# Optimization experiments

Measured on AMD Instinct MI355X. Metric: run time of the kernel, lower is better.

## Reference

```python
import jax, jax.numpy as jnp
import numpy as np

B, L, D, N = 4, 8192, 1024, 16


def setup_inputs() -> dict:
    key = jax.random.key(0)
    ks = jax.random.split(key, 6)
    x = jax.random.normal(ks[0], (B, L, D), dtype=jnp.float32)
    Wd = jax.random.normal(ks[1], (D, D), dtype=jnp.float32) / np.sqrt(D).astype(np.float32)
    bd = jnp.zeros((D,), dtype=jnp.float32)
    Wb = jax.random.normal(ks[2], (N, D), dtype=jnp.float32) / np.sqrt(D).astype(np.float32)
    bb = jnp.zeros((N,), dtype=jnp.float32)
    Wc = jax.random.normal(ks[3], (N, D), dtype=jnp.float32) / np.sqrt(D).astype(np.float32)
    bc = jnp.zeros((N,), dtype=jnp.float32)
    # A_log = log(rand*0.9 + 0.1) as in the torch init
    A_log = jnp.log(jax.random.uniform(ks[4], (D, N), dtype=jnp.float32) * 0.9 + 0.1)
    D_param = jnp.ones((D,), dtype=jnp.float32)
    return {"x": x, "Wd": Wd, "bd": bd, "Wb": Wb, "bb": bb,
            "Wc": Wc, "bc": bc, "A_log": A_log, "D_param": D_param}


def _ssm(x, Wd, bd, Wb, bb, Wc, bc, A_log, D_param):
    # Projections over the full sequence (batched GEMMs)
    delta = jax.nn.softplus(jnp.einsum('bld,ed->ble', x, Wd) + bd)   # [B,L,D]
    Bm = jnp.einsum('bld,nd->bln', x, Wb) + bb                       # [B,L,N]
    Cm = jnp.einsum('bld,nd->bln', x, Wc) + bc                       # [B,L,N]
    A = -jnp.exp(A_log)                                              # [D,N]

    h0 = jnp.zeros((x.shape[0], x.shape[2], A_log.shape[1]), dtype=x.dtype)  # [B,D,N]

    def step(h, inp):
        x_t, d_t, b_t, c_t = inp  # [B,D],[B,D],[B,N],[B,N]
        bar_A = jnp.exp(jnp.minimum(d_t[..., None] * A, 2.0))                 # [B,D,N]
        bar_B = jnp.clip(d_t[..., None] * b_t[:, None, :], -2.0, 2.0)         # [B,D,N]
        h = jnp.clip(bar_A * h + bar_B * x_t[..., None], -100.0, 100.0)       # [B,D,N]
        y_t = jnp.sum(h * c_t[:, None, :], axis=-1) + x_t * D_param           # [B,D]
        return h, y_t

    xs = (jnp.swapaxes(x, 0, 1), jnp.swapaxes(delta, 0, 1),
          jnp.swapaxes(Bm, 0, 1), jnp.swapaxes(Cm, 0, 1))  # time-major [L,B,*]
    _, ys = jax.lax.scan(step, h0, xs)  # ys: [L,B,D]
    return jnp.swapaxes(ys, 0, 1)       # [B,L,D]


def reference(x, Wd, bd, Wb, bb, Wc, bc, A_log, D_param):
    return _ssm(x, Wd, bd, Wb, bb, Wc, bc, A_log, D_param)
```

## Files before the change

### kernel.cpp

```cpp
#include <hip/hip_runtime.h>
#include <hip/hip_bf16.h>
#include <cstdint>
#include <cstddef>


#define LOG2E 1.44269504088896340736f

typedef short bf16x8 __attribute__((ext_vector_type(8)));
typedef float f32x4 __attribute__((ext_vector_type(4)));

#if __has_builtin(__builtin_amdgcn_exp2f)
#define EXP2F(x) __builtin_amdgcn_exp2f(x)
#else
#define EXP2F(x) exp2f(x)
#endif

static constexpr int B_ = 4;
static constexpr int L_ = 8192;
static constexpr int CHUNKS = 32;
static constexpr int CHUNK = L_ / CHUNKS;
static constexpr int WARM = 128;


__global__ void cvt_x_kernel(const float* __restrict__ x, __hip_bfloat16* __restrict__ xb) {
    size_t i = ((size_t)blockIdx.x * blockDim.x + threadIdx.x) * 4;
    float4 v = *(const float4*)(x + i);
    __hip_bfloat16* p = xb + i;
    p[0] = __float2bfloat16(v.x);
    p[1] = __float2bfloat16(v.y);
    p[2] = __float2bfloat16(v.z);
    p[3] = __float2bfloat16(v.w);
}

__global__ void prep_wall_kernel(const float* __restrict__ Wd, const float* __restrict__ Wb,
                                 const float* __restrict__ Wc, __hip_bfloat16* __restrict__ Wall) {
    int gid = blockIdx.x * blockDim.x + threadIdx.x;
    size_t idx = (size_t)gid * 4;
    int row = (int)(idx >> 10);
    int k = (int)(idx & 1023);
    __hip_bfloat16* p = Wall + idx;
    const float* src = nullptr;
    if (row < 1024) src = Wd + (size_t)row * 1024 + k;
    else if (row < 1040) src = Wb + (size_t)(row - 1024) * 1024 + k;
    else if (row < 1056) src = Wc + (size_t)(row - 1040) * 1024 + k;
    if (src) {
        float4 v = *(const float4*)src;
        p[0] = __float2bfloat16(v.x);
        p[1] = __float2bfloat16(v.y);
        p[2] = __float2bfloat16(v.z);
        p[3] = __float2bfloat16(v.w);
    } else {
        __hip_bfloat16 z = __float2bfloat16(0.0f);
        p[0] = z; p[1] = z; p[2] = z; p[3] = z;
    }
}


__global__ __launch_bounds__(256) void gemm_kernel(
    const __hip_bfloat16* __restrict__ X, const __hip_bfloat16* __restrict__ W,
    const float* __restrict__ bd, const float* __restrict__ bb, const float* __restrict__ bc,
    __hip_bfloat16* __restrict__ deltab, float* __restrict__ Bm, float* __restrict__ Cm) {
    __shared__ short smem[128 * 144];
    short* As = smem;
    short* Bs = smem + 128 * 64;
    const int bm = blockIdx.x;
    const int bn = blockIdx.y;
    const int t = threadIdx.x;
    const int lane = t & 63;
    const int wave = t >> 6;
    const int wm = (wave >> 1) * 64;
    const int wn = (wave & 1) * 64;
    const int rowS = t >> 3;
    const int kbS = t & 7;

    f32x4 acc[4][4];
#pragma unroll
    for (int i = 0; i < 4; ++i)
#pragma unroll
        for (int j = 0; j < 4; ++j) {
            f32x4 z = {0.f, 0.f, 0.f, 0.f};
            acc[i][j] = z;
        }

    const size_t Abase = (size_t)bm * 128 * 1024;
    const size_t Bbase = (size_t)bn * 128 * 1024;

    for (int kt = 0; kt < 16; ++kt) {
        __syncthreads();
#pragma unroll
        for (int r = 0; r < 4; ++r) {
            int row = r * 32 + rowS;
            int kb = kbS ^ (row & 7);
            const __hip_bfloat16* ga = X + Abase + (size_t)row * 1024 + kt * 64 + kb * 8;
            const __hip_bfloat16* gb = W + Bbase + (size_t)row * 1024 + kt * 64 + kb * 8;
            __builtin_amdgcn_global_load_lds(
                (const __attribute__((address_space(1))) unsigned int*)ga,
                (__attribute__((address_space(3))) unsigned int*)&As[(r * 256 + t) * 8], 16, 0, 0);
            __builtin_amdgcn_global_load_lds(
                (const __attribute__((address_space(1))) unsigned int*)gb,
                (__attribute__((address_space(3))) unsigned int*)&Bs[(r * 256 + t) * 8], 16, 0, 0);
        }
        __syncthreads();
#pragma unroll
        for (int ks = 0; ks < 2; ++ks) {
            bf16x8 af[4], bfr[4];
#pragma unroll
            for (int i = 0; i < 4; ++i) {
                int m = wm + i * 16 + (lane & 15);
                int kb = (ks * 4 + (lane >> 4)) ^ (m & 7);
                af[i] = *(const bf16x8*)&As[m * 64 + kb * 8];
            }
#pragma unroll
            for (int j = 0; j < 4; ++j) {
                int n = wn + j * 16 + (lane & 15);
                int kb = (ks * 4 + (lane >> 4)) ^ (n & 7);
                bfr[j] = *(const bf16x8*)&Bs[n * 64 + kb * 8];
            }
#pragma unroll
            for (int i = 0; i < 4; ++i)
#pragma unroll
                for (int j = 0; j < 4; ++j)
                    acc[i][j] = __builtin_amdgcn_mfma_f32_16x16x32_bf16(af[i], bfr[j], acc[i][j], 0, 0, 0);
        }
    }

    const int rquad = lane >> 4;
    const int cl = lane & 15;
    if (bn < 8) {
        __syncthreads();
#pragma unroll
        for (int i = 0; i < 4; ++i) {
            int row0 = wm + i * 16 + rquad * 4;
#pragma unroll
            for (int j = 0; j < 4; ++j) {
                int col_l = wn + j * 16 + cl;
                float bv = bd[bn * 128 + col_l];
#pragma unroll
                for (int r = 0; r < 4; ++r) {
                    float z = acc[i][j][r] + bv;
                    float sp = fmaxf(z, 0.f) + __logf(1.f + __expf(-fabsf(z)));
                    __hip_bfloat16 hb = __float2bfloat16(sp);
                    smem[(row0 + r) * 144 + col_l] = *(short*)&hb;
                }
            }
        }
        __syncthreads();
        const int rloc = t >> 4;
        const int seg = t & 15;
#pragma unroll
        for (int p = 0; p < 8; ++p) {
            int row_l = p * 16 + rloc;
            bf16x8 v = *(const bf16x8*)&smem[row_l * 144 + seg * 8];
            *(bf16x8*)(deltab + (size_t)(bm * 128 + row_l) * 1024 + bn * 128 + seg * 8) = v;
        }
    } else {
#pragma unroll
        for (int i = 0; i < 4; ++i) {
            int mrow = bm * 128 + wm + i * 16 + rquad * 4;
#pragma unroll
            for (int j = 0; j < 4; ++j) {
                int cloc = wn + j * 16 + cl;
                if (cloc < 16) {
                    float bv = bb[cloc];
#pragma unroll
                    for (int r = 0; r < 4; ++r)
                        Bm[(size_t)(mrow + r) * 16 + cloc] = acc[i][j][r] + bv;
                } else if (cloc < 32) {
                    float bv = bc[cloc - 16];
#pragma unroll
                    for (int r = 0; r < 4; ++r)
                        Cm[(size_t)(mrow + r) * 16 + (cloc - 16)] = acc[i][j][r] + bv;
                }
            }
        }
    }
}


__global__ __launch_bounds__(256) void scan_kernel(
    const __hip_bfloat16* __restrict__ deltab, const __hip_bfloat16* __restrict__ xb,
    const float* __restrict__ Bmg, const float* __restrict__ Cmg,
    const float* __restrict__ A_log, const float* __restrict__ Dparam,
    float* __restrict__ y) {
    const int bid = blockIdx.x;
    const int dblk = bid & 3;
    const int c = (bid >> 2) & 31;
    const int b = bid >> 7;
    const int d = dblk * 256 + threadIdx.x;

    float A2[16];
#pragma unroll
    for (int n = 0; n < 16; ++n)
        A2[n] = -__expf(A_log[d * 16 + n]) * LOG2E;
    const float Dp = Dparam[d];

    float h[16];
#pragma unroll
    for (int n = 0; n < 16; ++n) h[n] = 0.f;

    const int lmain = c * CHUNK;
    const int warm = (c == 0) ? 0 : WARM;
    const int l0 = lmain - warm;
    const size_t baseBL = (size_t)b * L_;

    const __hip_bfloat16* dptr = deltab + (baseBL + l0) * 1024 + d;
    const __hip_bfloat16* xptr = xb + (baseBL + l0) * 1024 + d;
    const float* bcp = Bmg + (baseBL + l0) * 16;
    const float* ccp = Cmg + (baseBL + l0) * 16;
    float* yptr = y + (baseBL + lmain) * 1024 + d;

    float dl[4], xv[4];
#pragma unroll
    for (int u = 0; u < 4; ++u) {
        dl[u] = __bfloat162float(dptr[(size_t)u * 1024]);
        xv[u] = __bfloat162float(xptr[(size_t)u * 1024]);
    }
    dptr += 4096; xptr += 4096;
    f32x4 bs[4], cs[4];
#pragma unroll
    for (int q = 0; q < 4; ++q) {
        bs[q] = *(const f32x4*)(bcp + q * 4);
        cs[q] = *(const f32x4*)(ccp + q * 4);
    }
    bcp += 16; ccp += 16;

    const int nb = (warm + CHUNK) >> 2;
    const int wb = warm >> 2;
    for (int body = 0; body < nb; ++body) {
        float dln[4], xvn[4];
#pragma unroll
        for (int u = 0; u < 4; ++u) {
            dln[u] = __bfloat162float(dptr[(size_t)u * 1024]);
            xvn[u] = __bfloat162float(xptr[(size_t)u * 1024]);
        }
        dptr += 4096; xptr += 4096;
        const bool emit = body >= wb;
#pragma unroll
        for (int u = 0; u < 4; ++u) {
            f32x4 bn_[4], cn_[4];
#pragma unroll
            for (int q = 0; q < 4; ++q) {
                bn_[q] = *(const f32x4*)(bcp + q * 4);
                cn_[q] = *(const f32x4*)(ccp + q * 4);
            }
            bcp += 16; ccp += 16;
            const float dlt = dl[u], xu = xv[u];
            float yacc = xu * Dp;
#pragma unroll
            for (int n = 0; n < 16; ++n) {
                float a = EXP2F(dlt * A2[n]);
                float bB = __builtin_amdgcn_fmed3f(dlt * bs[n >> 2][n & 3], -2.f, 2.f);
                float hn = __builtin_amdgcn_fmed3f(fmaf(a, h[n], bB * xu), -100.f, 100.f);
                h[n] = hn;
                yacc = fmaf(hn, cs[n >> 2][n & 3], yacc);
            }
            if (emit) yptr[(size_t)u * 1024] = yacc;
#pragma unroll
            for (int q = 0; q < 4; ++q) { bs[q] = bn_[q]; cs[q] = cn_[q]; }
        }
        if (emit) yptr += 4096;
#pragma unroll
        for (int u = 0; u < 4; ++u) { dl[u] = dln[u]; xv[u] = xvn[u]; }
    }
}


extern "C" void kernel_launch(void* const* d_in, const int* in_sizes, int n_in,
                              void* d_out, int out_size, void* d_ws, size_t ws_size,
                              hipStream_t stream) {
    const float* x      = (const float*)d_in[0];
    const float* Wd     = (const float*)d_in[1];
    const float* bd     = (const float*)d_in[2];
    const float* Wb     = (const float*)d_in[3];
    const float* bb     = (const float*)d_in[4];
    const float* Wc     = (const float*)d_in[5];
    const float* bc     = (const float*)d_in[6];
    const float* A_log  = (const float*)d_in[7];
    const float* Dparam = (const float*)d_in[8];
    float* y = (float*)d_out;

    char* ws = (char*)d_ws;
    float* Bm              = (float*)(ws);
    float* Cm              = (float*)(ws + 2097152);
    __hip_bfloat16* xb     = (__hip_bfloat16*)(ws + 4194304);
    __hip_bfloat16* deltab = (__hip_bfloat16*)(ws + 71303168);
    __hip_bfloat16* Wall   = (__hip_bfloat16*)(ws + 138412032);

    cvt_x_kernel<<<32768, 256, 0, stream>>>(x, xb);
    prep_wall_kernel<<<1152, 256, 0, stream>>>(Wd, Wb, Wc, Wall);
    gemm_kernel<<<dim3(256, 9), 256, 0, stream>>>(xb, Wall, bd, bb, bc, deltab, Bm, Cm);
    scan_kernel<<<512, 256, 0, stream>>>(deltab, xb, Bm, Cm, A_log, Dparam, y);
}
```

Before: 589.4 us.

## Split scan state across four lanes per channel with packed FMA and DPP reduction

The scan kernel now gives each channel four threads, each holding 4 of the 16 state elements, so the grid grows from 512 to 2048 blocks. Per-timestep math uses two-wide packed float FMAs, and the partial y sums are combined across the four lanes with DPP swizzles, with one lane writing the output. This is meant to raise occupancy and shorten each thread's serial dependency chain in a latency-bound recurrence. The cost is four redundant loads of delta and x per channel, cross-lane reduction work, and lower coalescing for the y stores.

```diff
diff --git a/kernel.cpp b/kernel.cpp
--- a/kernel.cpp
+++ b/kernel.cpp
@@ -8,12 +8,24 @@
 
 typedef short bf16x8 __attribute__((ext_vector_type(8)));
 typedef float f32x4 __attribute__((ext_vector_type(4)));
+typedef float f32x2 __attribute__((ext_vector_type(2)));
 
 #if __has_builtin(__builtin_amdgcn_exp2f)
 #define EXP2F(x) __builtin_amdgcn_exp2f(x)
 #else
 #define EXP2F(x) exp2f(x)
 #endif
+
+static __device__ __forceinline__ f32x2 pk_fma2(f32x2 a, f32x2 b, f32x2 c) {
+#if __has_builtin(__builtin_elementwise_fma)
+    return __builtin_elementwise_fma(a, b, c);
+#else
+    f32x2 r;
+    r.x = fmaf(a.x, b.x, c.x);
+    r.y = fmaf(a.y, b.y, c.y);
+    return r;
+#endif
+}
 
 static constexpr int B_ = 4;
 static constexpr int L_ = 8192;
@@ -177,26 +189,30 @@
 }
 
 
-__global__ __launch_bounds__(256) void scan_kernel(
+__global__ __launch_bounds__(256, 8) void scan_kernel(
     const __hip_bfloat16* __restrict__ deltab, const __hip_bfloat16* __restrict__ xb,
     const float* __restrict__ Bmg, const float* __restrict__ Cmg,
     const float* __restrict__ A_log, const float* __restrict__ Dparam,
     float* __restrict__ y) {
     const int bid = blockIdx.x;
-    const int dblk = bid & 3;
-    const int c = (bid >> 2) & 31;
-    const int b = bid >> 7;
-    const int d = dblk * 256 + threadIdx.x;
-
-    float A2[16];
-#pragma unroll
-    for (int n = 0; n < 16; ++n)
-        A2[n] = -__expf(A_log[d * 16 + n]) * LOG2E;
+    const int dblk = bid & 15;
+    const int c = (bid >> 4) & 31;
+    const int b = bid >> 9;
+    const int t = threadIdx.x;
+    const int nq = t & 3;
+    const int d = dblk * 64 + (t >> 2);
+    const int n0 = nq * 4;
+
+    f32x2 A2p[2];
+#pragma unroll
+    for (int q = 0; q < 2; ++q) {
+        A2p[q].x = -__expf(A_log[d * 16 + n0 + 2 * q]) * LOG2E;
+        A2p[q].y = -__expf(A_log[d * 16 + n0 + 2 * q + 1]) * LOG2E;
+    }
     const float Dp = Dparam[d];
 
-    float h[16];
-#pragma unroll
-    for (int n = 0; n < 16; ++n) h[n] = 0.f;
+    f32x2 h0 = {0.f, 0.f};
+    f32x2 h1 = {0.f, 0.f};
 
     const int lmain = c * CHUNK;
     const int warm = (c == 0) ? 0 : WARM;
@@ -205,8 +221,8 @@
 
     const __hip_bfloat16* dptr = deltab + (baseBL + l0) * 1024 + d;
     const __hip_bfloat16* xptr = xb + (baseBL + l0) * 1024 + d;
-    const float* bcp = Bmg + (baseBL + l0) * 16;
-    const float* ccp = Cmg + (baseBL + l0) * 16;
+    const float* bcp = Bmg + (baseBL + l0) * 16 + n0;
+    const float* ccp = Cmg + (baseBL + l0) * 16 + n0;
     float* yptr = y + (baseBL + lmain) * 1024 + d;
 
     float dl[4], xv[4];
@@ -216,12 +232,8 @@
         xv[u] = __bfloat162float(xptr[(size_t)u * 1024]);
     }
     dptr += 4096; xptr += 4096;
-    f32x4 bs[4], cs[4];
-#pragma unroll
-    for (int q = 0; q < 4; ++q) {
-        bs[q] = *(const f32x4*)(bcp + q * 4);
-        cs[q] = *(const f32x4*)(ccp + q * 4);
-    }
+    f32x4 bs = *(const f32x4*)bcp;
+    f32x4 cs = *(const f32x4*)ccp;
     bcp += 16; ccp += 16;
 
     const int nb = (warm + CHUNK) >> 2;
@@ -237,27 +249,44 @@
         const bool emit = body >= wb;
 #pragma unroll
         for (int u = 0; u < 4; ++u) {
-            f32x4 bn_[4], cn_[4];
-#pragma unroll
-            for (int q = 0; q < 4; ++q) {
-                bn_[q] = *(const f32x4*)(bcp + q * 4);
-                cn_[q] = *(const f32x4*)(ccp + q * 4);
-            }
-            bcp += 16; ccp += 16;
+            f32x4 bn_ = *(const f32x4*)(bcp + (size_t)u * 16);
+            f32x4 cn_ = *(const f32x4*)(ccp + (size_t)u * 16);
             const float dlt = dl[u], xu = xv[u];
-            float yacc = xu * Dp;
-#pragma unroll
-            for (int n = 0; n < 16; ++n) {
-                float a = EXP2F(dlt * A2[n]);
-                float bB = __builtin_amdgcn_fmed3f(dlt * bs[n >> 2][n & 3], -2.f, 2.f);
-                float hn = __builtin_amdgcn_fmed3f(fmaf(a, h[n], bB * xu), -100.f, 100.f);
-                h[n] = hn;
-                yacc = fmaf(hn, cs[n >> 2][n & 3], yacc);
-            }
-            if (emit) yptr[(size_t)u * 1024] = yacc;
+            const f32x2 dlt2 = {dlt, dlt};
+            const f32x2 xu2 = {xu, xu};
+            f32x2 tA0 = dlt2 * A2p[0];
+            f32x2 tA1 = dlt2 * A2p[1];
+            f32x2 a0 = {EXP2F(tA0.x), EXP2F(tA0.y)};
+            f32x2 a1 = {EXP2F(tA1.x), EXP2F(tA1.y)};
+            f32x2 blo = {bs[0], bs[1]};
+            f32x2 bhi = {bs[2], bs[3]};
+            f32x2 tB0 = dlt2 * blo;
+            f32x2 tB1 = dlt2 * bhi;
+            tB0.x = __builtin_amdgcn_fmed3f(tB0.x, -2.f, 2.f);
+            tB0.y = __builtin_amdgcn_fmed3f(tB0.y, -2.f, 2.f);
+            tB1.x = __builtin_amdgcn_fmed3f(tB1.x, -2.f, 2.f);
+            tB1.y = __builtin_amdgcn_fmed3f(tB1.y, -2.f, 2.f);
+            h0 = pk_fma2(a0, h0, tB0 * xu2);
+            h1 = pk_fma2(a1, h1, tB1 * xu2);
+            h0.x = __builtin_amdgcn_fmed3f(h0.x, -100.f, 100.f);
+            h0.y = __builtin_amdgcn_fmed3f(h0.y, -100.f, 100.f);
+            h1.x = __builtin_amdgcn_fmed3f(h1.x, -100.f, 100.f);
+            h1.y = __builtin_amdgcn_fmed3f(h1.y, -100.f, 100.f);
+            if (emit) {
+                f32x2 clo = {cs[0], cs[1]};
+                f32x2 chi = {cs[2], cs[3]};
+                f32x2 y2 = pk_fma2(h1, chi, h0 * clo);
+                float yl = y2.x + y2.y;
+                yl += __int_as_float(__builtin_amdgcn_update_dpp(
+                    0, __float_as_int(yl), 0xB1, 0xF, 0xF, true));
+                yl += __int_as_float(__builtin_amdgcn_update_dpp(
+                    0, __float_as_int(yl), 0x4E, 0xF, 0xF, true));
+                if (nq == 0) yptr[(size_t)u * 1024] = fmaf(xu, Dp, yl);
+            }
 #pragma unroll
             for (int q = 0; q < 4; ++q) { bs[q] = bn_[q]; cs[q] = cn_[q]; }
         }
+        bcp += 64; ccp += 64;
         if (emit) yptr += 4096;
 #pragma unroll
         for (int u = 0; u < 4; ++u) { dl[u] = dln[u]; xv[u] = xvn[u]; }
@@ -289,5 +318,5 @@
     cvt_x_kernel<<<32768, 256, 0, stream>>>(x, xb);
     prep_wall_kernel<<<1152, 256, 0, stream>>>(Wd, Wb, Wc, Wall);
     gemm_kernel<<<dim3(256, 9), 256, 0, stream>>>(xb, Wall, bd, bb, bc, deltab, Bm, Cm);
-    scan_kernel<<<512, 256, 0, stream>>>(deltab, xb, Bm, Cm, A_log, Dparam, y);
-}
+    scan_kernel<<<2048, 256, 0, stream>>>(deltab, xb, Bm, Cm, A_log, Dparam, y);
+}
```

Result: slower. 615.2 us (+4.4%).
